# Kernel optimization log

Hardware: AMD Instinct MI355X
Metric: run time of the kernel (lower is better)

## Reference

```python
import jax, jax.numpy as jnp
import numpy as np

# Hard-coded dims from the module
D, L, R, H, M, T = 64, 90, 5760, 1024, 1024, 20
N_OUT = 3
B = 64  # per-timestep batch; feature has B*T rows


def setup_inputs() -> dict:
    key = jax.random.key(0)
    ks = jax.random.split(key, 20)
    def w(i, shape, fan_in):
        return jax.random.normal(ks[i], shape, dtype=jnp.float32) * (1.0 / np.sqrt(fan_in))
    return {
        "feature": jax.random.normal(ks[0], (B * T, L, D), dtype=jnp.float32),
        # additive attention params (alpha over L locations)
        "attn_Wx": w(1, (D, D), D),
        "attn_Wh": w(2, (H, D), H),
        "attn_v": w(3, (D,), D),
        # LSTM (PyTorch gate order i,f,g,o)
        "W_ih": w(4, (4 * H, R), R),
        "W_hh": w(5, (4 * H, H), H),
        "b_ih": jnp.zeros((4 * H,), jnp.float32),
        "b_hh": jnp.zeros((4 * H,), jnp.float32),
        # output head
        "Wh_w": w(6, (M, H), H),
        "Wh_b": jnp.zeros((M,), jnp.float32),
        "Wy_w": w(7, (M, R), R),
        "Wu_w": w(8, (N_OUT, M), M),
        "Wu_b": jnp.zeros((N_OUT,), jnp.float32),
        # LSTM-state initializers
        "iWh_w": w(9, (H, D), D),
        "iWh_b": jnp.zeros((H,), jnp.float32),
        "iWc_w": w(10, (H, D), D),
        "iWc_b": jnp.zeros((H,), jnp.float32),
    }


def reference(feature, attn_Wx, attn_Wh, attn_v, W_ih, W_hh, b_ih, b_hh,
              Wh_w, Wh_b, Wy_w, Wu_w, Wu_b, iWh_w, iWh_b, iWc_w, iWc_b):
    batch = feature.shape[0] // T
    seq = feature.reshape(batch, T, L, D).transpose(1, 0, 2, 3)  # [T,B,L,D]

    # initializeLSTM (no_grad in the original -> stop_gradient)
    f0 = jnp.mean(seq[0], axis=1)                                  # [B,D]
    h0 = jax.lax.stop_gradient(jnp.tanh(f0 @ iWh_w.T + iWh_b))     # [B,H]
    c0 = jax.lax.stop_gradient(jnp.tanh(f0 @ iWc_w.T + iWc_b))     # [B,H]

    def step(carry, xt):  # xt: [B,L,D]
        h, c = carry
        # additive attention over L locations
        e = jnp.tanh(jnp.einsum('bld,da->bla', xt, attn_Wx)
                     + (h @ attn_Wh)[:, None, :]) @ attn_v          # [B,L]
        alpha = jax.nn.softmax(e, axis=1)
        visual = (xt * alpha[:, :, None]).reshape(-1, R)            # [B,R]
        # single LSTM step (PyTorch gate order i,f,g,o)
        gates = visual @ W_ih.T + b_ih + h @ W_hh.T + b_hh          # [B,4H]
        i, f, g, o = jnp.split(gates, 4, axis=-1)
        c = jax.nn.sigmoid(f) * c + jax.nn.sigmoid(i) * jnp.tanh(g)
        h = jax.nn.sigmoid(o) * jnp.tanh(c)
        # ut = Wu(Wh(h) + Wy(visual)); dropout omitted for determinism
        ut = (h @ Wh_w.T + Wh_b + visual @ Wy_w.T) @ Wu_w.T + Wu_b  # [B,n_out]
        return (h, c), ut

    _, outs = jax.lax.scan(step, (h0, c0), seq)                     # [T,B,n_out]
    return outs.transpose(1, 0, 2).reshape(batch * T, -1)
```

## Files before the change

kernel.cpp:

```cpp
#include <hip/hip_runtime.h>
#include <math.h>

typedef _Float16 half8 __attribute__((ext_vector_type(8)));
typedef _Float16 half4v __attribute__((ext_vector_type(4)));
typedef _Float16 half2v __attribute__((ext_vector_type(2)));
typedef float floatx16 __attribute__((ext_vector_type(16)));
typedef float floatx4 __attribute__((ext_vector_type(4)));

#define TT 20
#define NB 64
#define LL 90
#define DD 64
#define RR 5760
#define HH 1024
#define NG 4096
#define KT 6784
#define CH0 90
#define CHT 106

__device__ __forceinline__ float sigm(float x) { return 1.f / (1.f + expf(-x)); }

__global__ __launch_bounds__(256) void k_conv(const float* __restrict__ s,
                                              _Float16* __restrict__ d, int n) {
    int i = (blockIdx.x * 256 + threadIdx.x) * 4;
    if (i + 4 <= n) {
        const float4 v = *(const float4*)(s + i);
        half4v o;
        o[0] = (_Float16)v.x; o[1] = (_Float16)v.y;
        o[2] = (_Float16)v.z; o[3] = (_Float16)v.w;
        *(half4v*)(d + i) = o;
    } else {
        for (; i < n; ++i) d[i] = (_Float16)s[i];
    }
}

__global__ __launch_bounds__(256) void k_init(const float* __restrict__ feat,
        const float* __restrict__ iWh_w, const float* __restrict__ iWh_b,
        const float* __restrict__ iWc_w, const float* __restrict__ iWc_b,
        float* __restrict__ h, float* __restrict__ c, _Float16* __restrict__ h16) {
    __shared__ float f0p[4][DD];
    __shared__ float f0[DD];
    const int b = blockIdx.x, tid = threadIdx.x;
    const int dd = tid & 63, lg = tid >> 6;
    const float* frow = feat + (size_t)(b * TT) * RR;
    float p = 0;
    for (int l = lg; l < LL; l += 4) p += frow[l * DD + dd];
    f0p[lg][dd] = p;
    __syncthreads();
    if (tid < DD) f0[tid] = (f0p[0][tid] + f0p[1][tid] + f0p[2][tid] + f0p[3][tid]) * (1.0f / LL);
    __syncthreads();
    for (int o = tid; o < HH; o += 256) {
        float ah = iWh_b[o], ac = iWc_b[o];
        for (int d0 = 0; d0 < DD; d0 += 4) {
            const float4 wh = *(const float4*)(iWh_w + (size_t)o * DD + d0);
            const float4 wc = *(const float4*)(iWc_w + (size_t)o * DD + d0);
            ah += f0[d0] * wh.x + f0[d0 + 1] * wh.y + f0[d0 + 2] * wh.z + f0[d0 + 3] * wh.w;
            ac += f0[d0] * wc.x + f0[d0 + 1] * wc.y + f0[d0 + 2] * wc.z + f0[d0 + 3] * wc.w;
        }
        const float hv = tanhf(ah), cv = tanhf(ac);
        h[b * HH + o] = hv; c[b * HH + o] = cv;
        h16[b * HH + o] = (_Float16)hv;
    }
}

__global__ __launch_bounds__(512) void k_step(int tattn, int do_cell,
        const float* __restrict__ gpart, const float* __restrict__ b_ih,
        const float* __restrict__ b_hh, float* __restrict__ cbuf,
        _Float16* __restrict__ h16, _Float16* __restrict__ H16,
        const float* __restrict__ h0buf, const float* __restrict__ feat,
        const _Float16* __restrict__ WxTg, const float* __restrict__ Wh,
        const float* __restrict__ v, _Float16* __restrict__ V16) {
    __shared__ float sf[RR];
    __shared__ _Float16 x16[96 * DD];
    __shared__ _Float16 wxT[DD * DD];
    __shared__ float sh[HH];
    __shared__ float hWhp[8][DD];
    __shared__ float hWh[DD];
    __shared__ float sv[DD];
    __shared__ float se[128];
    __shared__ float red[128];
    __shared__ float salpha[LL];
    const int b = blockIdx.x, tid = threadIdx.x;
    const int t = tattn;
    if (tid < DD) sv[tid] = v[tid];

    if (t < TT) {
        const float* frow = feat + ((size_t)b * TT + t) * RR;
        for (int e = tid * 4; e < RR; e += 2048) {
            const float4 u = *(const float4*)(frow + e);
            *(float4*)(sf + e) = u;
            half4v o;
            o[0] = (_Float16)u.x; o[1] = (_Float16)u.y;
            o[2] = (_Float16)u.z; o[3] = (_Float16)u.w;
            *(half4v*)(x16 + e) = o;
        }
        if (tid < 48) *(half8*)(x16 + RR + tid * 8) = half8{0,0,0,0,0,0,0,0};
        *(half8*)(wxT + tid * 8) = *(const half8*)(WxTg + tid * 8);
    }

    if (do_cell) {
        const int j0 = tid * 2;
        float ag[4][2];
#pragma unroll
        for (int g = 0; g < 4; ++g) { ag[g][0] = 0.f; ag[g][1] = 0.f; }
#pragma unroll
        for (int sp = 0; sp < 4; ++sp) {
            const float* P = gpart + ((size_t)sp * NB + b) * NG;
#pragma unroll
            for (int g = 0; g < 4; ++g) {
                const float2 pv = *(const float2*)(P + g * HH + j0);
                ag[g][0] += pv.x; ag[g][1] += pv.y;
            }
        }
#pragma unroll
        for (int g = 0; g < 4; ++g) {
            const float2 bi = *(const float2*)(b_ih + g * HH + j0);
            const float2 bh = *(const float2*)(b_hh + g * HH + j0);
            ag[g][0] += bi.x + bh.x; ag[g][1] += bi.y + bh.y;
        }
        const float2 cold = *(const float2*)(cbuf + (size_t)b * HH + j0);
        float co[2] = { cold.x, cold.y };
        float2 cnew; half2v hh2;
#pragma unroll
        for (int q = 0; q < 2; ++q) {
            const float cv = sigm(ag[1][q]) * co[q] + sigm(ag[0][q]) * tanhf(ag[2][q]);
            const float hv = sigm(ag[3][q]) * tanhf(cv);
            ((float*)&cnew)[q] = cv;
            hh2[q] = (_Float16)hv;
            sh[j0 + q] = hv;
        }
        *(float2*)(cbuf + (size_t)b * HH + j0) = cnew;
        *(half2v*)(h16 + (size_t)b * HH + j0) = hh2;
        *(half2v*)(H16 + ((size_t)(t - 1) * NB + b) * HH + j0) = hh2;
    } else {
        for (int e = tid; e < HH; e += 512) sh[e] = h0buf[(size_t)b * HH + e];
    }
    __syncthreads();
    if (t >= TT) return;

    { const int a = tid & 63, q = tid >> 6;
      const float* Wq = Wh + (size_t)(q * 128) * DD + a;
      const float* shq = sh + q * 128;
      float p0 = 0.f, p1 = 0.f;
#pragma unroll 8
      for (int k = 0; k < 128; k += 2) {
          p0 += shq[k] * Wq[(size_t)k * DD];
          p1 += shq[k + 1] * Wq[(size_t)(k + 1) * DD];
      }
      hWhp[q][a] = p0 + p1; }
    __syncthreads();
    if (tid < DD) {
        float s = 0.f;
#pragma unroll
        for (int q = 0; q < 8; ++q) s += hWhp[q][tid];
        hWh[tid] = s;
    }
    if (tid < 128) se[tid] = -1e30f;
    __syncthreads();

    { const int w = tid >> 6, ln = tid & 63;
      if (w < 6) {
          const int l0 = w * 16, c = ln & 15, g = ln >> 4;
          float es[4] = {0.f, 0.f, 0.f, 0.f};
#pragma unroll
          for (int at = 0; at < 4; ++at) {
              floatx4 acc = {0.f, 0.f, 0.f, 0.f};
#pragma unroll
              for (int kk = 0; kk < 2; ++kk) {
                  const half8 af = *(const half8*)(x16 + (l0 + c) * DD + g * 8 + kk * 32);
                  const half8 bf = *(const half8*)(wxT + (at * 16 + c) * DD + g * 8 + kk * 32);
                  acc = __builtin_amdgcn_mfma_f32_16x16x32_f16(af, bf, acc, 0, 0, 0);
              }
#pragma unroll
              for (int q = 0; q < 4; ++q) {
                  const int aa = at * 16 + c;
                  es[q] += tanhf(acc[q] + hWh[aa]) * sv[aa];
              }
          }
#pragma unroll
          for (int q = 0; q < 4; ++q) {
              es[q] += __shfl_xor(es[q], 1, 64);
              es[q] += __shfl_xor(es[q], 2, 64);
              es[q] += __shfl_xor(es[q], 4, 64);
              es[q] += __shfl_xor(es[q], 8, 64);
          }
          if (c == 0) {
#pragma unroll
              for (int q = 0; q < 4; ++q) {
                  const int l = l0 + g * 4 + q;
                  if (l < LL) se[l] = es[q];
              }
          }
      } }
    __syncthreads();

    if (tid < 128) red[tid] = se[tid];
    __syncthreads();
    for (int s = 64; s; s >>= 1) { if (tid < s) red[tid] = fmaxf(red[tid], red[tid + s]); __syncthreads(); }
    const float mx = red[0];
    __syncthreads();
    float ex = 0.f;
    if (tid < LL) { ex = expf(se[tid] - mx); salpha[tid] = ex; }
    if (tid < 128) red[tid] = ex;
    __syncthreads();
    for (int s = 64; s; s >>= 1) { if (tid < s) red[tid] += red[tid + s]; __syncthreads(); }
    const float inv = 1.f / red[0];
    __syncthreads();
    if (tid < LL) salpha[tid] *= inv;
    __syncthreads();

    _Float16* vout = V16 + ((size_t)t * NB + b) * RR;
    for (int e = tid * 4; e < RR; e += 2048) {
        const float4 u4 = *(const float4*)(sf + e);
        const float al = salpha[e >> 6];
        half4v o;
        o[0] = (_Float16)(u4.x * al); o[1] = (_Float16)(u4.y * al);
        o[2] = (_Float16)(u4.z * al); o[3] = (_Float16)(u4.w * al);
        *(half4v*)(vout + e) = o;
    }
}

__device__ __forceinline__ void stage_tile(const char* src, size_t stride, char* lds, int ln) {
    const char* g = src + (size_t)(ln >> 3) * stride + (((ln & 7) ^ (ln >> 3)) << 4);
#pragma unroll
    for (int i = 0; i < 8; ++i)
        __builtin_amdgcn_global_load_lds(
            (const __attribute__((address_space(1))) void*)(g + (size_t)(i * 8) * stride),
            (__attribute__((address_space(3))) void*)(lds + i * 1024), 16, 0, 0);
}

struct Src2 { const char* p0; size_t s0; const char* p1; size_t s1; };

__device__ __forceinline__ const char* chunk_ptr(const Src2& s, int c, size_t& stride) {
    if (c < CH0) { stride = s.s0; return s.p0 + (size_t)c * 128; }
    stride = s.s1; return s.p1 + (size_t)(c - CH0) * 128;
}

template<int NT, int SB>
__global__ __launch_bounds__(128) void k_gemm(
        const _Float16* __restrict__ A0, const _Float16* __restrict__ A1,
        const _Float16* __restrict__ B0, const _Float16* __restrict__ B1,
        float* __restrict__ C, int ldc, size_t part_elems) {
    __shared__ char smem[65536];
    const int bid = blockIdx.x;
    const int kb = bid % SB;
    const int nt = (bid / SB) % NT;
    const int mt = bid / (SB * NT);
    const int tid = threadIdx.x, w = tid >> 6, ln = tid & 63;
    char* wlds = smem + w * 32768;

    const int arow = mt * 64, brow = nt * 64;
    Src2 As = { (const char*)(A0 + (size_t)arow * RR), (size_t)RR * 2,
                (const char*)(A1 + (size_t)arow * HH), (size_t)HH * 2 };
    Src2 Bs = { (const char*)(B0 + (size_t)brow * RR), (size_t)RR * 2,
                (const char*)(B1 + (size_t)brow * HH), (size_t)HH * 2 };

    floatx16 acc00, acc01, acc10, acc11;
#pragma unroll
    for (int i = 0; i < 16; ++i) { acc00[i] = 0.f; acc01[i] = 0.f; acc10[i] = 0.f; acc11[i] = 0.f; }

    const int start = kb * 2 + w;
    const int STRIDE = SB * 2;
    const int r = ln & 31;
    const int xsw = (r & 7) << 4;
    const int fo = (ln >> 5) * 16;
    const int rbyte = r * 128;

    int c = start, bsel = 0;
    { size_t st; const char* p = chunk_ptr(As, c, st); stage_tile(p, st, wlds, ln);
      p = chunk_ptr(Bs, c, st); stage_tile(p, st, wlds + 8192, ln); }
    while (true) {
        const int cn = c + STRIDE;
        if (cn < CHT) {
            char* nl = wlds + ((bsel ^ 1) << 14);
            size_t st; const char* p = chunk_ptr(As, cn, st); stage_tile(p, st, nl, ln);
            p = chunk_ptr(Bs, cn, st); stage_tile(p, st, nl + 8192, ln);
            asm volatile("s_waitcnt vmcnt(16)" ::: "memory");
        } else {
            asm volatile("s_waitcnt vmcnt(0)" ::: "memory");
        }
        __builtin_amdgcn_sched_barrier(0);
        const char* LA = wlds + (bsel << 14);
        const char* LB = LA + 8192;
#pragma unroll
        for (int kk = 0; kk < 4; ++kk) {
            const int o = ((kk * 32 + fo) ^ xsw);
            const half8 a0 = *(const half8*)(LA + rbyte + o);
            const half8 a1 = *(const half8*)(LA + 4096 + rbyte + o);
            const half8 b0 = *(const half8*)(LB + rbyte + o);
            const half8 b1 = *(const half8*)(LB + 4096 + rbyte + o);
            acc00 = __builtin_amdgcn_mfma_f32_32x32x16_f16(a0, b0, acc00, 0, 0, 0);
            acc01 = __builtin_amdgcn_mfma_f32_32x32x16_f16(a0, b1, acc01, 0, 0, 0);
            acc10 = __builtin_amdgcn_mfma_f32_32x32x16_f16(a1, b0, acc10, 0, 0, 0);
            acc11 = __builtin_amdgcn_mfma_f32_32x32x16_f16(a1, b1, acc11, 0, 0, 0);
        }
        if (cn >= CHT) break;
        c = cn; bsel ^= 1;
    }
    __syncthreads();
    float* Rg = (float*)(smem + w * 16384);
    const int rbase = 4 * (ln >> 5), lr = ln & 31;
#pragma unroll
    for (int q = 0; q < 16; ++q) {
        const int row = rbase + (q & 3) + 8 * (q >> 2);
        Rg[row * 64 + lr]             = acc00[q];
        Rg[row * 64 + 32 + lr]        = acc01[q];
        Rg[(row + 32) * 64 + lr]      = acc10[q];
        Rg[(row + 32) * 64 + 32 + lr] = acc11[q];
    }
    __syncthreads();
    const float* R0 = (const float*)smem;
    const float* R1 = (const float*)(smem + 16384);
    float* Cout = C + (size_t)kb * part_elems;
    for (int e = tid * 4; e < 4096; e += 512) {
        const float4 u = *(const float4*)(R0 + e);
        const float4 v2 = *(const float4*)(R1 + e);
        float4 s2; s2.x = u.x + v2.x; s2.y = u.y + v2.y; s2.z = u.z + v2.z; s2.w = u.w + v2.w;
        const int row = e >> 6, col = e & 63;
        *(float4*)(Cout + (size_t)(arow + row) * ldc + brow + col) = s2;
    }
}

__global__ __launch_bounds__(256) void k_wfuse(const float* __restrict__ Wy,
        const float* __restrict__ Whw, const float* __restrict__ Wu,
        const float* __restrict__ Whb, const float* __restrict__ Wub,
        _Float16* __restrict__ Wyu16, float* __restrict__ cst,
        const float* __restrict__ Wx, _Float16* __restrict__ WxT) {
    const int tid = threadIdx.x;
    if (blockIdx.x == CHT + 1) {
        const int a = tid >> 2, k0 = (tid & 3) * 16;
#pragma unroll
        for (int j = 0; j < 16; ++j)
            WxT[(size_t)a * DD + k0 + j] = (_Float16)Wx[(size_t)(k0 + j) * DD + a];
        return;
    }
    __shared__ float sWu[3 * HH];
    __shared__ float part[4][3][64];
    for (int e = tid * 4; e < 3 * HH; e += 1024)
        *(float4*)(sWu + e) = *(const float4*)(Wu + e);
    __syncthreads();
    if (blockIdx.x == CHT) {
        float a0 = 0, a1 = 0, a2 = 0;
        for (int m = tid; m < HH; m += 256) {
            const float wb = Whb[m];
            a0 += sWu[m] * wb; a1 += sWu[HH + m] * wb; a2 += sWu[2 * HH + m] * wb;
        }
        __shared__ float rp[3][256];
        rp[0][tid] = a0; rp[1][tid] = a1; rp[2][tid] = a2;
        __syncthreads();
        for (int s = 128; s; s >>= 1) {
            if (tid < s) { rp[0][tid] += rp[0][tid + s]; rp[1][tid] += rp[1][tid + s]; rp[2][tid] += rp[2][tid + s]; }
            __syncthreads();
        }
        if (tid < 3) cst[tid] = rp[tid][0] + Wub[tid];
        return;
    }
    const int kk = tid & 63, qm = tid >> 6;
    const int k = blockIdx.x * 64 + kk;
    const float* src; size_t ld;
    if (blockIdx.x < CH0) { src = Wy + k; ld = RR; }
    else { src = Whw + (k - RR); ld = HH; }
    float a0 = 0, a1 = 0, a2 = 0;
    for (int m = qm * 256; m < qm * 256 + 256; ++m) {
        const float val = src[(size_t)m * ld];
        a0 += sWu[m] * val; a1 += sWu[HH + m] * val; a2 += sWu[2 * HH + m] * val;
    }
    part[qm][0][kk] = a0; part[qm][1][kk] = a1; part[qm][2][kk] = a2;
    __syncthreads();
    if (tid < 192) {
        const int j = tid >> 6, k2 = tid & 63;
        const float s = part[0][j][k2] + part[1][j][k2] + part[2][j][k2] + part[3][j][k2];
        Wyu16[(size_t)j * KT + blockIdx.x * 64 + k2] = (_Float16)s;
    }
}

__global__ __launch_bounds__(256) void k_final2(const _Float16* __restrict__ V16,
        const _Float16* __restrict__ H16, const _Float16* __restrict__ Wyu,
        const float* __restrict__ cst, float* __restrict__ out) {
    __shared__ float rp[4][3];
    const int r = blockIdx.x, tid = threadIdx.x;
    const _Float16* vrow = V16 + (size_t)r * RR;
    const _Float16* hrow = H16 + (size_t)r * HH;
    float a0 = 0, a1 = 0, a2 = 0;
    for (int e = tid * 8; e < KT; e += 2048) {
        half8 x;
        if (e < RR) x = *(const half8*)(vrow + e);
        else        x = *(const half8*)(hrow + (e - RR));
        const half8 w0 = *(const half8*)(Wyu + e);
        const half8 w1 = *(const half8*)(Wyu + KT + e);
        const half8 w2 = *(const half8*)(Wyu + 2 * KT + e);
#pragma unroll
        for (int i = 0; i < 8; ++i) {
            const float xv = (float)x[i];
            a0 += xv * (float)w0[i]; a1 += xv * (float)w1[i]; a2 += xv * (float)w2[i];
        }
    }
    for (int o = 32; o > 0; o >>= 1) {
        a0 += __shfl_down(a0, o, 64); a1 += __shfl_down(a1, o, 64); a2 += __shfl_down(a2, o, 64);
    }
    const int wv = tid >> 6;
    if ((tid & 63) == 0) { rp[wv][0] = a0; rp[wv][1] = a1; rp[wv][2] = a2; }
    __syncthreads();
    if (tid < 3) {
        const float x = rp[0][tid] + rp[1][tid] + rp[2][tid] + rp[3][tid] + cst[tid];
        const int b = r & 63, ts = r >> 6;
        out[((size_t)b * TT + ts) * 3 + tid] = x;
    }
}

extern "C" void kernel_launch(void* const* d_in, const int* in_sizes, int n_in,
                              void* d_out, int out_size, void* d_ws, size_t ws_size,
                              hipStream_t stream) {
    (void)in_sizes; (void)n_in; (void)out_size;
    const float* feature = (const float*)d_in[0];
    const float* attn_Wx = (const float*)d_in[1];
    const float* attn_Wh = (const float*)d_in[2];
    const float* attn_v  = (const float*)d_in[3];
    const float* W_ih    = (const float*)d_in[4];
    const float* W_hh    = (const float*)d_in[5];
    const float* b_ih    = (const float*)d_in[6];
    const float* b_hh    = (const float*)d_in[7];
    const float* Wh_w    = (const float*)d_in[8];
    const float* Wh_b    = (const float*)d_in[9];
    const float* Wy_w    = (const float*)d_in[10];
    const float* Wu_w    = (const float*)d_in[11];
    const float* Wu_b    = (const float*)d_in[12];
    const float* iWh_w   = (const float*)d_in[13];
    const float* iWh_b   = (const float*)d_in[14];
    const float* iWc_w   = (const float*)d_in[15];
    const float* iWc_b   = (const float*)d_in[16];
    float* out = (float*)d_out;

    char* ws = (char*)d_ws;
    size_t off = 0;
    auto alloc = [&](size_t bytes) { void* p = ws + off; off += (bytes + 255) & ~(size_t)255; return p; };
    _Float16* Wih16 = (_Float16*)alloc((size_t)NG * RR * 2);
    _Float16* Whh16 = (_Float16*)alloc((size_t)NG * HH * 2);
    _Float16* WxT16 = (_Float16*)alloc((size_t)DD * DD * 2);
    _Float16* V16   = (_Float16*)alloc((size_t)TT * NB * RR * 2);
    _Float16* H16   = (_Float16*)alloc((size_t)TT * NB * HH * 2);
    float*    hbuf  = (float*)alloc((size_t)NB * HH * 4);
    float*    cbuf  = (float*)alloc((size_t)NB * HH * 4);
    _Float16* h16   = (_Float16*)alloc((size_t)NB * HH * 2);
    float*    gpart = (float*)alloc((size_t)4 * NB * NG * 4);
    _Float16* Wyu16 = (_Float16*)alloc((size_t)3 * KT * 2);
    float*    cstb  = (float*)alloc(16);
    if (ws_size < off) return;

    k_conv<<<(NG * RR / 4 + 255) / 256, 256, 0, stream>>>(W_ih, Wih16, NG * RR);
    k_conv<<<(NG * HH / 4 + 255) / 256, 256, 0, stream>>>(W_hh, Whh16, NG * HH);
    k_wfuse<<<CHT + 2, 256, 0, stream>>>(Wy_w, Wh_w, Wu_w, Wh_b, Wu_b, Wyu16, cstb,
                                         attn_Wx, WxT16);
    k_init<<<64, 256, 0, stream>>>(feature, iWh_w, iWh_b, iWc_w, iWc_b, hbuf, cbuf, h16);

    k_step<<<64, 512, 0, stream>>>(0, 0, gpart, b_ih, b_hh, cbuf, h16, H16, hbuf,
                                   feature, WxT16, attn_Wh, attn_v, V16);
    for (int t = 0; t < TT; ++t) {
        const _Float16* Vt = V16 + (size_t)t * NB * RR;
        k_gemm<64, 4><<<256, 128, 0, stream>>>(Vt, h16, Wih16, Whh16,
                                               gpart, NG, (size_t)NB * NG);
        k_step<<<64, 512, 0, stream>>>(t + 1, 1, gpart, b_ih, b_hh, cbuf, h16, H16, hbuf,
                                       feature, WxT16, attn_Wh, attn_v, V16);
    }

    k_final2<<<1280, 256, 0, stream>>>(V16, H16, Wyu16, cstb, out);
}
```

Baseline: 573.2 us.

## Fuse output head projection into step kernel and merge weight conversion launches

The output head's dot products with the fused Wyu weights move into k_step: each block computes the visual and hidden partial dot products as it produces them, writes small per-step partials, and the last step assembles the output. This removes the separate k_final2 pass that re-read all stored V16 and H16 rows, and removes the H16 buffer entirely. The two fp16 weight conversion kernels are also merged into one launch. In exchange the latency-bound serial step kernel gains extra reduction work and Wyu reads on every step.

```diff
diff --git a/kernel.cpp b/kernel.cpp
--- a/kernel.cpp
+++ b/kernel.cpp
@@ -20,18 +20,18 @@
 
 __device__ __forceinline__ float sigm(float x) { return 1.f / (1.f + expf(-x)); }
 
-__global__ __launch_bounds__(256) void k_conv(const float* __restrict__ s,
-                                              _Float16* __restrict__ d, int n) {
+__global__ __launch_bounds__(256) void k_conv2(const float* __restrict__ s1, _Float16* __restrict__ d1, int n1,
+                                               const float* __restrict__ s2, _Float16* __restrict__ d2, int n2) {
     int i = (blockIdx.x * 256 + threadIdx.x) * 4;
-    if (i + 4 <= n) {
-        const float4 v = *(const float4*)(s + i);
-        half4v o;
-        o[0] = (_Float16)v.x; o[1] = (_Float16)v.y;
-        o[2] = (_Float16)v.z; o[3] = (_Float16)v.w;
-        *(half4v*)(d + i) = o;
-    } else {
-        for (; i < n; ++i) d[i] = (_Float16)s[i];
-    }
+    const float* s; _Float16* d;
+    if (i < n1) { s = s1 + i; d = d1 + i; }
+    else if ((i -= n1) < n2) { s = s2 + i; d = d2 + i; }
+    else return;
+    const float4 v = *(const float4*)s;
+    half4v o;
+    o[0] = (_Float16)v.x; o[1] = (_Float16)v.y;
+    o[2] = (_Float16)v.z; o[3] = (_Float16)v.w;
+    *(half4v*)d = o;
 }
 
 __global__ __launch_bounds__(256) void k_init(const float* __restrict__ feat,
@@ -66,10 +66,12 @@
 __global__ __launch_bounds__(512) void k_step(int tattn, int do_cell,
         const float* __restrict__ gpart, const float* __restrict__ b_ih,
         const float* __restrict__ b_hh, float* __restrict__ cbuf,
-        _Float16* __restrict__ h16, _Float16* __restrict__ H16,
-        const float* __restrict__ h0buf, const float* __restrict__ feat,
-        const _Float16* __restrict__ WxTg, const float* __restrict__ Wh,
-        const float* __restrict__ v, _Float16* __restrict__ V16) {
+        _Float16* __restrict__ h16, const float* __restrict__ h0buf,
+        const float* __restrict__ feat, const _Float16* __restrict__ WxTg,
+        const float* __restrict__ Wh, const float* __restrict__ v,
+        _Float16* __restrict__ V16, const _Float16* __restrict__ Wyu,
+        float* __restrict__ vpart, float* __restrict__ hpart,
+        const float* __restrict__ cst, float* __restrict__ out) {
     __shared__ float sf[RR];
     __shared__ _Float16 x16[96 * DD];
     __shared__ _Float16 wxT[DD * DD];
@@ -80,9 +82,13 @@
     __shared__ float se[128];
     __shared__ float red[128];
     __shared__ float salpha[LL];
+    __shared__ float hdr[8][6];
+    __shared__ float hloc[3];
     const int b = blockIdx.x, tid = threadIdx.x;
     const int t = tattn;
     if (tid < DD) sv[tid] = v[tid];
+    float hp0 = 0.f, hp1 = 0.f, hp2 = 0.f;
+    float vp0 = 0.f, vp1 = 0.f, vp2 = 0.f;
 
     if (t < TT) {
         const float* frow = feat + ((size_t)b * TT + t) * RR;
@@ -131,92 +137,133 @@
         }
         *(float2*)(cbuf + (size_t)b * HH + j0) = cnew;
         *(half2v*)(h16 + (size_t)b * HH + j0) = hh2;
-        *(half2v*)(H16 + ((size_t)(t - 1) * NB + b) * HH + j0) = hh2;
+        const float h0f = (float)hh2[0], h1f = (float)hh2[1];
+        hp0 = h0f * (float)Wyu[0 * KT + RR + j0] + h1f * (float)Wyu[0 * KT + RR + j0 + 1];
+        hp1 = h0f * (float)Wyu[1 * KT + RR + j0] + h1f * (float)Wyu[1 * KT + RR + j0 + 1];
+        hp2 = h0f * (float)Wyu[2 * KT + RR + j0] + h1f * (float)Wyu[2 * KT + RR + j0 + 1];
     } else {
         for (int e = tid; e < HH; e += 512) sh[e] = h0buf[(size_t)b * HH + e];
     }
     __syncthreads();
-    if (t >= TT) return;
-
-    { const int a = tid & 63, q = tid >> 6;
-      const float* Wq = Wh + (size_t)(q * 128) * DD + a;
-      const float* shq = sh + q * 128;
-      float p0 = 0.f, p1 = 0.f;
+
+    if (t < TT) {
+        { const int a = tid & 63, q = tid >> 6;
+          const float* Wq = Wh + (size_t)(q * 128) * DD + a;
+          const float* shq = sh + q * 128;
+          float p0 = 0.f, p1 = 0.f;
 #pragma unroll 8
-      for (int k = 0; k < 128; k += 2) {
-          p0 += shq[k] * Wq[(size_t)k * DD];
-          p1 += shq[k + 1] * Wq[(size_t)(k + 1) * DD];
-      }
-      hWhp[q][a] = p0 + p1; }
-    __syncthreads();
-    if (tid < DD) {
+          for (int k = 0; k < 128; k += 2) {
+              p0 += shq[k] * Wq[(size_t)k * DD];
+              p1 += shq[k + 1] * Wq[(size_t)(k + 1) * DD];
+          }
+          hWhp[q][a] = p0 + p1; }
+        __syncthreads();
+        if (tid < DD) {
+            float s = 0.f;
+#pragma unroll
+            for (int q = 0; q < 8; ++q) s += hWhp[q][tid];
+            hWh[tid] = s;
+        }
+        if (tid < 128) se[tid] = -1e30f;
+        __syncthreads();
+
+        { const int w = tid >> 6, ln = tid & 63;
+          if (w < 6) {
+              const int l0 = w * 16, c = ln & 15, g = ln >> 4;
+              float es[4] = {0.f, 0.f, 0.f, 0.f};
+#pragma unroll
+              for (int at = 0; at < 4; ++at) {
+                  floatx4 acc = {0.f, 0.f, 0.f, 0.f};
+#pragma unroll
+                  for (int kk = 0; kk < 2; ++kk) {
+                      const half8 af = *(const half8*)(x16 + (l0 + c) * DD + g * 8 + kk * 32);
+                      const half8 bf = *(const half8*)(wxT + (at * 16 + c) * DD + g * 8 + kk * 32);
+                      acc = __builtin_amdgcn_mfma_f32_16x16x32_f16(af, bf, acc, 0, 0, 0);
+                  }
+#pragma unroll
+                  for (int q = 0; q < 4; ++q) {
+                      const int aa = at * 16 + c;
+                      es[q] += tanhf(acc[q] + hWh[aa]) * sv[aa];
+                  }
+              }
+#pragma unroll
+              for (int q = 0; q < 4; ++q) {
+                  es[q] += __shfl_xor(es[q], 1, 64);
+                  es[q] += __shfl_xor(es[q], 2, 64);
+                  es[q] += __shfl_xor(es[q], 4, 64);
+                  es[q] += __shfl_xor(es[q], 8, 64);
+              }
+              if (c == 0) {
+#pragma unroll
+                  for (int q = 0; q < 4; ++q) {
+                      const int l = l0 + g * 4 + q;
+                      if (l < LL) se[l] = es[q];
+                  }
+              }
+          } }
+        __syncthreads();
+
+        if (tid < 128) red[tid] = se[tid];
+        __syncthreads();
+        for (int s = 64; s; s >>= 1) { if (tid < s) red[tid] = fmaxf(red[tid], red[tid + s]); __syncthreads(); }
+        const float mx = red[0];
+        __syncthreads();
+        float ex = 0.f;
+        if (tid < LL) { ex = expf(se[tid] - mx); salpha[tid] = ex; }
+        if (tid < 128) red[tid] = ex;
+        __syncthreads();
+        for (int s = 64; s; s >>= 1) { if (tid < s) red[tid] += red[tid + s]; __syncthreads(); }
+        const float inv = 1.f / red[0];
+        __syncthreads();
+        if (tid < LL) salpha[tid] *= inv;
+        __syncthreads();
+
+        _Float16* vout = V16 + ((size_t)t * NB + b) * RR;
+        for (int e = tid * 4; e < RR; e += 2048) {
+            const float4 u4 = *(const float4*)(sf + e);
+            const float al = salpha[e >> 6];
+            half4v o;
+            o[0] = (_Float16)(u4.x * al); o[1] = (_Float16)(u4.y * al);
+            o[2] = (_Float16)(u4.z * al); o[3] = (_Float16)(u4.w * al);
+            *(half4v*)(vout + e) = o;
+            const half4v w0 = *(const half4v*)(Wyu + e);
+            const half4v w1 = *(const half4v*)(Wyu + KT + e);
+            const half4v w2 = *(const half4v*)(Wyu + 2 * KT + e);
+#pragma unroll
+            for (int u = 0; u < 4; ++u) {
+                const float xv = (float)o[u];
+                vp0 += xv * (float)w0[u]; vp1 += xv * (float)w1[u]; vp2 += xv * (float)w2[u];
+            }
+        }
+    }
+
+    for (int o = 32; o; o >>= 1) {
+        hp0 += __shfl_down(hp0, o, 64); hp1 += __shfl_down(hp1, o, 64); hp2 += __shfl_down(hp2, o, 64);
+        vp0 += __shfl_down(vp0, o, 64); vp1 += __shfl_down(vp1, o, 64); vp2 += __shfl_down(vp2, o, 64);
+    }
+    if ((tid & 63) == 0) {
+        const int wv = tid >> 6;
+        hdr[wv][0] = hp0; hdr[wv][1] = hp1; hdr[wv][2] = hp2;
+        hdr[wv][3] = vp0; hdr[wv][4] = vp1; hdr[wv][5] = vp2;
+    }
+    __syncthreads();
+    if (tid < 6) {
         float s = 0.f;
 #pragma unroll
-        for (int q = 0; q < 8; ++q) s += hWhp[q][tid];
-        hWh[tid] = s;
-    }
-    if (tid < 128) se[tid] = -1e30f;
-    __syncthreads();
-
-    { const int w = tid >> 6, ln = tid & 63;
-      if (w < 6) {
-          const int l0 = w * 16, c = ln & 15, g = ln >> 4;
-          float es[4] = {0.f, 0.f, 0.f, 0.f};
-#pragma unroll
-          for (int at = 0; at < 4; ++at) {
-              floatx4 acc = {0.f, 0.f, 0.f, 0.f};
-#pragma unroll
-              for (int kk = 0; kk < 2; ++kk) {
-                  const half8 af = *(const half8*)(x16 + (l0 + c) * DD + g * 8 + kk * 32);
-                  const half8 bf = *(const half8*)(wxT + (at * 16 + c) * DD + g * 8 + kk * 32);
-                  acc = __builtin_amdgcn_mfma_f32_16x16x32_f16(af, bf, acc, 0, 0, 0);
-              }
-#pragma unroll
-              for (int q = 0; q < 4; ++q) {
-                  const int aa = at * 16 + c;
-                  es[q] += tanhf(acc[q] + hWh[aa]) * sv[aa];
-              }
-          }
-#pragma unroll
-          for (int q = 0; q < 4; ++q) {
-              es[q] += __shfl_xor(es[q], 1, 64);
-              es[q] += __shfl_xor(es[q], 2, 64);
-              es[q] += __shfl_xor(es[q], 4, 64);
-              es[q] += __shfl_xor(es[q], 8, 64);
-          }
-          if (c == 0) {
-#pragma unroll
-              for (int q = 0; q < 4; ++q) {
-                  const int l = l0 + g * 4 + q;
-                  if (l < LL) se[l] = es[q];
-              }
-          }
-      } }
-    __syncthreads();
-
-    if (tid < 128) red[tid] = se[tid];
-    __syncthreads();
-    for (int s = 64; s; s >>= 1) { if (tid < s) red[tid] = fmaxf(red[tid], red[tid + s]); __syncthreads(); }
-    const float mx = red[0];
-    __syncthreads();
-    float ex = 0.f;
-    if (tid < LL) { ex = expf(se[tid] - mx); salpha[tid] = ex; }
-    if (tid < 128) red[tid] = ex;
-    __syncthreads();
-    for (int s = 64; s; s >>= 1) { if (tid < s) red[tid] += red[tid + s]; __syncthreads(); }
-    const float inv = 1.f / red[0];
-    __syncthreads();
-    if (tid < LL) salpha[tid] *= inv;
-    __syncthreads();
-
-    _Float16* vout = V16 + ((size_t)t * NB + b) * RR;
-    for (int e = tid * 4; e < RR; e += 2048) {
-        const float4 u4 = *(const float4*)(sf + e);
-        const float al = salpha[e >> 6];
-        half4v o;
-        o[0] = (_Float16)(u4.x * al); o[1] = (_Float16)(u4.y * al);
-        o[2] = (_Float16)(u4.z * al); o[3] = (_Float16)(u4.w * al);
-        *(half4v*)(vout + e) = o;
+        for (int wv = 0; wv < 8; ++wv) s += hdr[wv][tid];
+        if (tid < 3) {
+            if (do_cell) { hpart[((size_t)(t - 1) * NB + b) * 3 + tid] = s; hloc[tid] = s; }
+        } else {
+            if (t < TT) vpart[((size_t)t * NB + b) * 3 + (tid - 3)] = s;
+        }
+    }
+    __syncthreads();
+    if (t == TT) {
+        for (int i = tid; i < TT * 3; i += 512) {
+            const int ts = i / 3, j = i - ts * 3;
+            const float hp = (ts == TT - 1) ? hloc[j] : hpart[((size_t)ts * NB + b) * 3 + j];
+            out[((size_t)b * TT + ts) * 3 + j] = vpart[((size_t)ts * NB + b) * 3 + j] + hp + cst[j];
+        }
     }
 }
 
@@ -371,40 +418,6 @@
         const int j = tid >> 6, k2 = tid & 63;
         const float s = part[0][j][k2] + part[1][j][k2] + part[2][j][k2] + part[3][j][k2];
         Wyu16[(size_t)j * KT + blockIdx.x * 64 + k2] = (_Float16)s;
-    }
-}
-
-__global__ __launch_bounds__(256) void k_final2(const _Float16* __restrict__ V16,
-        const _Float16* __restrict__ H16, const _Float16* __restrict__ Wyu,
-        const float* __restrict__ cst, float* __restrict__ out) {
-    __shared__ float rp[4][3];
-    const int r = blockIdx.x, tid = threadIdx.x;
-    const _Float16* vrow = V16 + (size_t)r * RR;
-    const _Float16* hrow = H16 + (size_t)r * HH;
-    float a0 = 0, a1 = 0, a2 = 0;
-    for (int e = tid * 8; e < KT; e += 2048) {
-        half8 x;
-        if (e < RR) x = *(const half8*)(vrow + e);
-        else        x = *(const half8*)(hrow + (e - RR));
-        const half8 w0 = *(const half8*)(Wyu + e);
-        const half8 w1 = *(const half8*)(Wyu + KT + e);
-        const half8 w2 = *(const half8*)(Wyu + 2 * KT + e);
-#pragma unroll
-        for (int i = 0; i < 8; ++i) {
-            const float xv = (float)x[i];
-            a0 += xv * (float)w0[i]; a1 += xv * (float)w1[i]; a2 += xv * (float)w2[i];
-        }
-    }
-    for (int o = 32; o > 0; o >>= 1) {
-        a0 += __shfl_down(a0, o, 64); a1 += __shfl_down(a1, o, 64); a2 += __shfl_down(a2, o, 64);
-    }
-    const int wv = tid >> 6;
-    if ((tid & 63) == 0) { rp[wv][0] = a0; rp[wv][1] = a1; rp[wv][2] = a2; }
-    __syncthreads();
-    if (tid < 3) {
-        const float x = rp[0][tid] + rp[1][tid] + rp[2][tid] + rp[3][tid] + cst[tid];
-        const int b = r & 63, ts = r >> 6;
-        out[((size_t)b * TT + ts) * 3 + tid] = x;
     }
 }
 
@@ -438,30 +451,32 @@
     _Float16* Whh16 = (_Float16*)alloc((size_t)NG * HH * 2);
     _Float16* WxT16 = (_Float16*)alloc((size_t)DD * DD * 2);
     _Float16* V16   = (_Float16*)alloc((size_t)TT * NB * RR * 2);
-    _Float16* H16   = (_Float16*)alloc((size_t)TT * NB * HH * 2);
     float*    hbuf  = (float*)alloc((size_t)NB * HH * 4);
     float*    cbuf  = (float*)alloc((size_t)NB * HH * 4);
     _Float16* h16   = (_Float16*)alloc((size_t)NB * HH * 2);
     float*    gpart = (float*)alloc((size_t)4 * NB * NG * 4);
     _Float16* Wyu16 = (_Float16*)alloc((size_t)3 * KT * 2);
+    float*    vpart = (float*)alloc((size_t)TT * NB * 3 * 4);
+    float*    hpart = (float*)alloc((size_t)TT * NB * 3 * 4);
     float*    cstb  = (float*)alloc(16);
     if (ws_size < off) return;
 
-    k_conv<<<(NG * RR / 4 + 255) / 256, 256, 0, stream>>>(W_ih, Wih16, NG * RR);
-    k_conv<<<(NG * HH / 4 + 255) / 256, 256, 0, stream>>>(W_hh, Whh16, NG * HH);
+    const int nconv = NG * RR + NG * HH;
+    k_conv2<<<(nconv / 4 + 255) / 256, 256, 0, stream>>>(W_ih, Wih16, NG * RR,
+                                                         W_hh, Whh16, NG * HH);
     k_wfuse<<<CHT + 2, 256, 0, stream>>>(Wy_w, Wh_w, Wu_w, Wh_b, Wu_b, Wyu16, cstb,
                                          attn_Wx, WxT16);
     k_init<<<64, 256, 0, stream>>>(feature, iWh_w, iWh_b, iWc_w, iWc_b, hbuf, cbuf, h16);
 
-    k_step<<<64, 512, 0, stream>>>(0, 0, gpart, b_ih, b_hh, cbuf, h16, H16, hbuf,
-                                   feature, WxT16, attn_Wh, attn_v, V16);
+    k_step<<<64, 512, 0, stream>>>(0, 0, gpart, b_ih, b_hh, cbuf, h16, hbuf,
+                                   feature, WxT16, attn_Wh, attn_v, V16, Wyu16,
+                                   vpart, hpart, cstb, out);
     for (int t = 0; t < TT; ++t) {
         const _Float16* Vt = V16 + (size_t)t * NB * RR;
         k_gemm<64, 4><<<256, 128, 0, stream>>>(Vt, h16, Wih16, Whh16,
                                                gpart, NG, (size_t)NB * NG);
-        k_step<<<64, 512, 0, stream>>>(t + 1, 1, gpart, b_ih, b_hh, cbuf, h16, H16, hbuf,
-                                       feature, WxT16, attn_Wh, attn_v, V16);
-    }
-
-    k_final2<<<1280, 256, 0, stream>>>(V16, H16, Wyu16, cstb, out);
-}
+        k_step<<<64, 512, 0, stream>>>(t + 1, 1, gpart, b_ih, b_hh, cbuf, h16, hbuf,
+                                       feature, WxT16, attn_Wh, attn_v, V16, Wyu16,
+                                       vpart, hpart, cstb, out);
+    }
+}
```

After: 613.6 us. 1.07x slower.
